# Performance work log

Measured on AMD Instinct MI355X. Metric: run time of the kernel, lower is better.

## Reference

```python
import jax, jax.numpy as jnp
import numpy as np

NB, T, NS, NC = 1024, 128, 12, 4
N = NS + NC  # stacked state+control dim


def setup_inputs() -> dict:
    key = jax.random.key(0)
    ks = jax.random.split(key, 7)
    x_init = jax.random.normal(ks[0], (NB, NS), jnp.float32)
    current_x = jax.random.normal(ks[1], (NB, T, NS), jnp.float32)
    current_u = jax.random.normal(ks[2], (NB, T, NC), jnp.float32)
    # symmetric positive-definite cost Hessian per (batch, t)
    G = 0.1 * jax.random.normal(ks[3], (NB, T, N, N), jnp.float32)
    Q = 0.5 * (G + jnp.swapaxes(G, -1, -2)) + jnp.eye(N, dtype=jnp.float32)
    p = jax.random.normal(ks[4], (NB, T, N), jnp.float32)
    # stable per-step dynamics linearizations
    A = 0.95 * jnp.eye(NS, dtype=jnp.float32) + 0.02 * jax.random.normal(ks[5], (NB, T, NS, NS), jnp.float32)
    Bmat = 0.1 * jax.random.normal(ks[6], (NB, T, NS, NC), jnp.float32)
    time = jnp.arange(T, dtype=jnp.int32)
    return {"x_init": x_init, "current_x": current_x, "current_u": current_u,
            "Q": Q, "p": p, "A": A, "Bmat": Bmat, "time": time}


def _lqr_backward(Q, p, A, Bmat):
    # time-major for scan: (T, NB, ...)
    Qs = jnp.moveaxis(Q, 1, 0)
    ps = jnp.moveaxis(p, 1, 0)
    As = jnp.moveaxis(A, 1, 0)
    Bs = jnp.moveaxis(Bmat, 1, 0)
    nb = Q.shape[0]
    V0 = jnp.zeros((nb, NS, NS), Q.dtype)  # V=0 reproduces the t==T-1 branch
    v0 = jnp.zeros((nb, NS), Q.dtype)

    def step(carry, inp):
        V, v = carry
        Qt0, pt, At, Bt = inp
        F = jnp.concatenate([At, Bt], axis=-1)          # (nb, ns, n)
        FT = jnp.swapaxes(F, -1, -2)                    # (nb, n, ns)
        Qt = Qt0 + FT @ V @ F                           # (nb, n, n)
        qt = pt + jnp.einsum('bsn,bs->bn', F, v)        # F^T v
        Qxx, Qxu = Qt[..., :NS, :NS], Qt[..., :NS, NS:]
        Qux, Quu = Qt[..., NS:, :NS], Qt[..., NS:, NS:]
        qx, qu = qt[..., :NS], qt[..., NS:]
        Quu_inv = jnp.linalg.pinv(Quu)                  # (nb, nc, nc)
        Kt = -(Quu_inv @ Qux)                           # (nb, nc, ns)
        kt = -jnp.einsum('bij,bj->bi', Quu_inv, qu)     # (nb, nc)
        KtT = jnp.swapaxes(Kt, -1, -2)
        Vn = Qxx + Qxu @ Kt + KtT @ Qux + KtT @ Quu @ Kt
        vn = (qx + jnp.einsum('bij,bj->bi', Qxu, kt)
              + jnp.einsum('bij,bj->bi', KtT, qu)
              + jnp.einsum('bij,bj->bi', KtT @ Quu, kt))
        return (Vn, vn), (Kt, kt)

    _, (K, k) = jax.lax.scan(step, (V0, v0), (Qs, ps, As, Bs), reverse=True)
    return jnp.moveaxis(K, 0, 1), jnp.moveaxis(k, 0, 1)


def _lqr_forward(x_init, current_u, Q, p, A, Bmat, K, k):
    Ks = jnp.moveaxis(K, 1, 0)
    ks_ = jnp.moveaxis(k, 1, 0)
    As = jnp.moveaxis(A, 1, 0)
    Bs = jnp.moveaxis(Bmat, 1, 0)
    cus = jnp.moveaxis(current_u, 1, 0)
    Qs = jnp.moveaxis(Q, 1, 0)
    ps = jnp.moveaxis(p, 1, 0)
    nb = x_init.shape[0]
    cost0 = jnp.zeros((nb,), x_init.dtype)

    def step(carry, inp):
        xt, cost = carry
        Kt, kt, At, Bt, cut, Qt, pt = inp
        # NOTE: original module never updates delta_x (stays zero), so delta_u == k_t
        ut = cut + kt
        xut = jnp.concatenate([xt, ut], axis=-1)        # (nb, n)
        xnext = jnp.einsum('bij,bj->bi', At, xt) + jnp.einsum('bij,bj->bi', Bt, ut)
        cost = cost + 0.5 * jnp.einsum('bi,bij,bj->b', xut, Qt, xut) + jnp.sum(xut * pt, axis=-1)
        return (xnext, cost), (xt, ut)

    (_, cost), (xs, us) = jax.lax.scan(step, (x_init, cost0), (Ks, ks_, As, Bs, cus, Qs, ps))
    # xs holds x_0..x_{T-1}, matching return of x[..., 0:-1, :]
    return jnp.moveaxis(xs, 0, 1), jnp.moveaxis(us, 0, 1), cost


def reference(x_init, current_x, current_u, Q, p, A, Bmat, time):
    K, k = _lqr_backward(Q, p, A, Bmat)
    return _lqr_forward(x_init, current_u, Q, p, A, Bmat, K, k)
```

## Files before the change

kernel.cpp:

```cpp
#include <hip/hip_runtime.h>


#define NBQ 1024
#define TT  128

__device__ __forceinline__ float dotf4(float4 a, float4 b) {
  return a.x*b.x + a.y*b.y + a.z*b.z + a.w*b.w;
}
__device__ __forceinline__ float dpp_qx1(float x) {
  return __int_as_float(__builtin_amdgcn_mov_dpp(__float_as_int(x), 0xB1, 0xF, 0xF, true));
}
__device__ __forceinline__ float dpp_qx2(float x) {
  return __int_as_float(__builtin_amdgcn_mov_dpp(__float_as_int(x), 0x4E, 0xF, 0xF, true));
}
template<int Q> __device__ __forceinline__ float4 bcast4(float4 v) {
  float4 r;
  r.x = __int_as_float(__builtin_amdgcn_mov_dpp(__float_as_int(v.x), Q*0x55, 0xF, 0xF, true));
  r.y = __int_as_float(__builtin_amdgcn_mov_dpp(__float_as_int(v.y), Q*0x55, 0xF, 0xF, true));
  r.z = __int_as_float(__builtin_amdgcn_mov_dpp(__float_as_int(v.z), Q*0x55, 0xF, 0xF, true));
  r.w = __int_as_float(__builtin_amdgcn_mov_dpp(__float_as_int(v.w), Q*0x55, 0xF, 0xF, true));
  return r;
}

#define MKS(K, O, MY)  { float4 mk_ = bcast4<O>(MY);                           \
  qt4_.x += gk_[K]*mk_.x; qt4_.y += gk_[K]*mk_.y;                              \
  qt4_.z += gk_[K]*mk_.z; qt4_.w += gk_[K]*mk_.w; }

#define BW_BODY(T_, QV, PV, CV, P0,P1,P2,P3, S0,S1,S2,S3)                      \
{                                                                              \
  const int  t_   = (T_);                                                      \
  const long bt_  = b*TT + t_;                                                 \
  const long btL_ = b*TT + ((t_ >= 4) ? (t_ - 4) : 0);                         \
  float4 qN_ = *(const float4*)(Qg + btL_*256 + qoff);                         \
  const float* fpL_ = lt48 ? (Ag + btL_*144 + l) : (Bg + btL_*48 + bm_);       \
  float fN0_ = fpL_[0], fN1_ = fpL_[fstr_], fN2_ = fpL_[2*fstr_], fN3_ = fpL_[foff3];  \
  float  pN_ = pg[btL_*16 + j];                                                \
  float  cN_ = cug[btL_*4 + q4];                                               \
  float* FTc_ = (t_ & 1) ? FT1 : FT0;                                          \
  float* FTn_ = (t_ & 1) ? FT0 : FT1;                                          \
                     \
  if (lt48)      { FTn_[ba] = P0; FTn_[ba+4] = P1; FTn_[ba+8] = P2; }          \
  else if (lt60) { FTn_[bb] = P0; FTn_[bb+3] = P1; FTn_[bb+6] = P2; FTn_[bb+9] = P3; } \
   \
  const float4* fj4_ = (const float4*)(FTc_ + j*12);                           \
  float4 f0_=fj4_[0], f1_=fj4_[1], f2_=fj4_[2];                                \
  const float4* vrow_ = (const float4*)(Vs + (3*r + dmin)*12);                 \
  float4 mv0_=vrow_[0], mv1_=vrow_[1], mv2_=vrow_[2];                          \
  float4 mw_ = *(const float4*)(vvS + 4*dmin);                                 \
                                      \
  float m0_, m1_, m2_;                                                         \
  { float4 r0_=bcast4<0>(mv0_), r1_=bcast4<0>(mv1_), r2_=bcast4<0>(mv2_);      \
    m0_ = dotf4(r0_,f0_)+dotf4(r1_,f1_)+dotf4(r2_,f2_); }                      \
  { float4 r0_=bcast4<1>(mv0_), r1_=bcast4<1>(mv1_), r2_=bcast4<1>(mv2_);      \
    m1_ = dotf4(r0_,f0_)+dotf4(r1_,f1_)+dotf4(r2_,f2_); }                      \
  { float4 r0_=bcast4<2>(mv0_), r1_=bcast4<2>(mv1_), r2_=bcast4<2>(mv2_);      \
    m2_ = dotf4(r0_,f0_)+dotf4(r1_,f1_)+dotf4(r2_,f2_); }                      \
  msh[(3*r+0)*16 + j] = m0_;                                                   \
  msh[(3*r+1)*16 + j] = m1_;                                                   \
  msh[(3*r+2)*16 + j] = m2_;                                                   \
                \
  float qtv_;                                                                  \
  { float4 w0_=bcast4<0>(mw_), w1_=bcast4<1>(mw_), w2_=bcast4<2>(mw_);         \
    qtv_ = PV + dotf4(w0_,f0_)+dotf4(w1_,f1_)+dotf4(w2_,f2_); }                \
                    \
  float gk_[12] = {f0_.x,f0_.y,f0_.z,f0_.w, f1_.x,f1_.y,f1_.z,f1_.w,           \
                   f2_.x,f2_.y,f2_.z,f2_.w};                                   \
  float4 mys0_ = *(const float4*)(msh + (3*q4+0)*16 + cb4);                    \
  float4 mys1_ = *(const float4*)(msh + (3*q4+1)*16 + cb4);                    \
  float4 mys2_ = *(const float4*)(msh + (3*q4+2)*16 + cb4);                    \
  float4 qt4_ = QV;                                                            \
  MKS(0,0,mys0_) MKS(1,0,mys1_) MKS(2,0,mys2_)                                 \
  MKS(3,1,mys0_) MKS(4,1,mys1_) MKS(5,1,mys2_)                                 \
  MKS(6,2,mys0_) MKS(7,2,mys1_) MKS(8,2,mys2_)                                 \
  MKS(9,3,mys0_) MKS(10,3,mys1_) MKS(11,3,mys2_)                               \
                                            \
  if (j >= 12)           *(float4*)(UxS + (j-12)*16 + cb4) = qt4_;             \
  if (cb == 3 && j < 12) *(float4*)(XuS + j*4) = qt4_;                         \
  if (l >= 12 && l < 16) quS[l-12] = qtv_;                                     \
                                         \
  float4 myquu_ = *(const float4*)(UxS + q4*16 + 12);                          \
  float4 myux_  = *(const float4*)(UxS + q4*16 + cb4);                         \
  float4 quv_   = *(const float4*)quS;                                         \
  float4 xr_    = *(const float4*)(XuS + jc*4);                                \
  float mm_[16];                                                               \
  { float4 t0_=bcast4<0>(myquu_); mm_[0]=t0_.x; mm_[1]=t0_.y; mm_[2]=t0_.z; mm_[3]=t0_.w; \
    float4 t1_=bcast4<1>(myquu_); mm_[4]=t1_.x; mm_[5]=t1_.y; mm_[6]=t1_.z; mm_[7]=t1_.w; \
    float4 t2_=bcast4<2>(myquu_); mm_[8]=t2_.x; mm_[9]=t2_.y; mm_[10]=t2_.z; mm_[11]=t2_.w; \
    float4 t3_=bcast4<3>(myquu_); mm_[12]=t3_.x; mm_[13]=t3_.y; mm_[14]=t3_.z; mm_[15]=t3_.w; } \
  float4 ux0_=bcast4<0>(myux_), ux1_=bcast4<1>(myux_),                         \
         ux2_=bcast4<2>(myux_), ux3_=bcast4<3>(myux_);                         \
                                       \
  float rdp_ = 1.0f/(mm_[0]*mm_[5] - mm_[1]*mm_[1]);                           \
  float pi00_ = mm_[5]*rdp_, pi01_ = -mm_[1]*rdp_, pi11_ = mm_[0]*rdp_;        \
  float w00_ = pi00_*mm_[2] + pi01_*mm_[6];                                    \
  float w01_ = pi00_*mm_[3] + pi01_*mm_[7];                                    \
  float w10_ = pi01_*mm_[2] + pi11_*mm_[6];                                    \
  float w11_ = pi01_*mm_[3] + pi11_*mm_[7];                                    \
  float t00_ = mm_[10] - (mm_[2]*w00_ + mm_[6]*w10_);                          \
  float t01_ = mm_[11] - (mm_[2]*w01_ + mm_[6]*w11_);                          \
  float t11_ = mm_[15] - (mm_[3]*w01_ + mm_[7]*w11_);                          \
  float rdt_ = 1.0f/(t00_*t11_ - t01_*t01_);                                   \
  float ti00_ = t11_*rdt_, ti01_ = -t01_*rdt_, ti11_ = t00_*rdt_;              \
  float u00_ = -(w00_*ti00_ + w01_*ti01_);                                     \
  float u01_ = -(w00_*ti01_ + w01_*ti11_);                                     \
  float u10_ = -(w10_*ti00_ + w11_*ti01_);                                     \
  float u11_ = -(w10_*ti01_ + w11_*ti11_);                                     \
  float i00_ = pi00_ - (u00_*w00_ + u01_*w01_);                                \
  float i01_ = pi01_ - (u00_*w10_ + u01_*w11_);                                \
  float i11_ = pi11_ - (u10_*w10_ + u11_*w11_);                                \
  float inv_[16] = { i00_, i01_, u00_, u01_,                                   \
                     i01_, i11_, u10_, u11_,                                   \
                     u00_, u10_, ti00_, ti01_,                                 \
                     u01_, u11_, ti01_, ti11_ };                               \
  float kt0_ = -(inv_[0] *quv_.x + inv_[1] *quv_.y + inv_[2] *quv_.z + inv_[3] *quv_.w); \
  float kt1_ = -(inv_[4] *quv_.x + inv_[5] *quv_.y + inv_[6] *quv_.z + inv_[7] *quv_.w); \
  float kt2_ = -(inv_[8] *quv_.x + inv_[9] *quv_.y + inv_[10]*quv_.z + inv_[11]*quv_.w); \
  float kt3_ = -(inv_[12]*quv_.x + inv_[13]*quv_.y + inv_[14]*quv_.z + inv_[15]*quv_.w); \
  float4 kc_[4];                                                               \
  _Pragma("unroll")                                                            \
  for (int c_ = 0; c_ < 4; ++c_) {                                             \
    kc_[c_].x = -(inv_[c_*4+0]*ux0_.x + inv_[c_*4+1]*ux1_.x + inv_[c_*4+2]*ux2_.x + inv_[c_*4+3]*ux3_.x); \
    kc_[c_].y = -(inv_[c_*4+0]*ux0_.y + inv_[c_*4+1]*ux1_.y + inv_[c_*4+2]*ux2_.y + inv_[c_*4+3]*ux3_.y); \
    kc_[c_].z = -(inv_[c_*4+0]*ux0_.z + inv_[c_*4+1]*ux1_.z + inv_[c_*4+2]*ux2_.z + inv_[c_*4+3]*ux3_.z); \
    kc_[c_].w = -(inv_[c_*4+0]*ux0_.w + inv_[c_*4+1]*ux1_.w + inv_[c_*4+2]*ux2_.w + inv_[c_*4+3]*ux3_.w); \
  }                                                                            \
  if (j < 12) {                                                                \
    float4 vn4_;                                                               \
    vn4_.x = qt4_.x + xr_.x*kc_[0].x + xr_.y*kc_[1].x + xr_.z*kc_[2].x + xr_.w*kc_[3].x; \
    vn4_.y = qt4_.y + xr_.x*kc_[0].y + xr_.y*kc_[1].y + xr_.z*kc_[2].y + xr_.w*kc_[3].y; \
    vn4_.z = qt4_.z + xr_.x*kc_[0].z + xr_.y*kc_[1].z + xr_.z*kc_[2].z + xr_.w*kc_[3].z; \
    vn4_.w = qt4_.w + xr_.x*kc_[0].w + xr_.y*kc_[1].w + xr_.z*kc_[2].w + xr_.w*kc_[3].w; \
    if (cb < 3) *(float4*)(Vs + j*12 + cb4) = vn4_;                            \
  }                                                                            \
  if (l < 12)                                                                  \
    vvS[l] = qtv_ + xr_.x*kt0_ + xr_.y*kt1_ + xr_.z*kt2_ + xr_.w*kt3_;         \
  float uv_ = CV + ((q4==0)?kt0_:(q4==1)?kt1_:(q4==2)?kt2_:kt3_);              \
  if (l < 4) { us_out[bt_*4 + l] = uv_; uL[t_*4 + l] = uv_; }                  \
  QV = qN_; S0 = fN0_; S1 = fN1_; S2 = fN2_; S3 = fN3_; PV = pN_; CV = cN_;    \
}

__global__ __launch_bounds__(64, 1) void lqr_fused(
    const float* __restrict__ Qg, const float* __restrict__ pg,
    const float* __restrict__ Ag, const float* __restrict__ Bg,
    const float* __restrict__ cug, const float* __restrict__ xinit,
    float* __restrict__ out)
{
  __shared__ __align__(16) float lds[1376];
  float* FT0 = lds;
  float* FT1 = lds + 192;
  float* Vs  = lds + 384;
  float* vvS = lds + 528;
  float* msh = lds + 544;
  float* UxS = lds + 736;
  float* XuS = lds + 800;
  float* quS = lds + 848;
  float* uL  = lds + 864;

  const int l    = threadIdx.x;
  const int j    = l & 15;
  const int r    = l >> 4;
  const int q4   = l & 3;
  const int cb   = l >> 4;
  const int cb4  = cb << 2;
  const int dmin = (q4 < 2) ? q4 : 2;
  const int jc   = (j < 12) ? j : 11;
  const long b   = blockIdx.x;
  const bool lt48 = (l < 48);
  const bool lt60 = (l < 60);
  const int  bm_  = lt48 ? 0 : ((l - 48) % 12);
  const int  fstr_ = lt48 ? 48 : 12;
  const int  foff3 = lt48 ? 96 : 36;
  const int  ba = (l % 12) * 12 + l / 12;
  const int  bb = 144 + ((l - 48) & 3) * 12 + ((l - 48) >> 2);
  const int  qoff = j * 16 + cb4;

  float* xs_out = out;
  float* us_out = out + (long)NBQ*TT*12;
  float* c_out  = out + (long)NBQ*TT*12 + (long)NBQ*TT*4;

  if (j < 12 && cb < 3) *(float4*)(Vs + j*12 + cb4) = make_float4(0.f,0.f,0.f,0.f);
  if (l < 12) vvS[l] = 0.f;

  const long base = b*TT;
  float4 q3v,q2v,q1v,q0v;
  float  p3v,c3v,p2v,c2v,p1v,c1v,p0v,c0v;
  float  f3a,f3b,f3c,f3d, f2a,f2b,f2c,f2d, f1a,f1b,f1c,f1d, f0a,f0b,f0c,f0d;
  {
    long bt;
    bt = base+127; q3v=*(const float4*)(Qg+bt*256+qoff); p3v=pg[bt*16+j]; c3v=cug[bt*4+q4];
    { const float* fp = lt48 ? (Ag+bt*144+l) : (Bg+bt*48+bm_);
      f3a=fp[0]; f3b=fp[fstr_]; f3c=fp[2*fstr_]; f3d=fp[foff3]; }
    bt = base+126; q2v=*(const float4*)(Qg+bt*256+qoff); p2v=pg[bt*16+j]; c2v=cug[bt*4+q4];
    { const float* fp = lt48 ? (Ag+bt*144+l) : (Bg+bt*48+bm_);
      f2a=fp[0]; f2b=fp[fstr_]; f2c=fp[2*fstr_]; f2d=fp[foff3]; }
    bt = base+125; q1v=*(const float4*)(Qg+bt*256+qoff); p1v=pg[bt*16+j]; c1v=cug[bt*4+q4];
    { const float* fp = lt48 ? (Ag+bt*144+l) : (Bg+bt*48+bm_);
      f1a=fp[0]; f1b=fp[fstr_]; f1c=fp[2*fstr_]; f1d=fp[foff3]; }
    bt = base+124; q0v=*(const float4*)(Qg+bt*256+qoff); p0v=pg[bt*16+j]; c0v=cug[bt*4+q4];
    { const float* fp = lt48 ? (Ag+bt*144+l) : (Bg+bt*48+bm_);
      f0a=fp[0]; f0b=fp[fstr_]; f0c=fp[2*fstr_]; f0d=fp[foff3]; }
  }
  if (lt48)      { FT1[ba] = f3a; FT1[ba+4] = f3b; FT1[ba+8] = f3c; }
  else if (lt60) { FT1[bb] = f3a; FT1[bb+3] = f3b; FT1[bb+6] = f3c; FT1[bb+9] = f3d; }

  #pragma unroll 1
  for (int tb = TT-1; tb >= 3; tb -= 4) {
    BW_BODY(tb,   q3v, p3v, c3v,  f2a,f2b,f2c,f2d,  f3a,f3b,f3c,f3d)
    BW_BODY(tb-1, q2v, p2v, c2v,  f1a,f1b,f1c,f1d,  f2a,f2b,f2c,f2d)
    BW_BODY(tb-2, q1v, p1v, c1v,  f0a,f0b,f0c,f0d,  f1a,f1b,f1c,f1d)
    BW_BODY(tb-3, q0v, p0v, c0v,  f3a,f3b,f3c,f3d,  f0a,f0b,f0c,f0d)
  }

  const int i4  = l >> 2;
  const int c0f = q4 << 2;
  const int i4c = (i4 < 12) ? i4 : 11;
  const int sl0 = (c0f+0)<<2, sl1 = (c0f+1)<<2, sl2 = (c0f+2)<<2, sl3 = (c0f+3)<<2;
  float s = xinit[b*12 + i4c];
  float cacc = 0.f;

  const long bt0 = base;
  float4 qfA = *(const float4*)(Qg + bt0*256 + 4*l);
  float4 ffA = (q4 < 3) ? *(const float4*)(Ag + bt0*144 + i4c*12 + c0f)
                        : *(const float4*)(Bg + bt0*48  + i4c*4);
  float  pfA = pg[bt0*16 + i4];
  float4 qfB = *(const float4*)(Qg + (bt0+1)*256 + 4*l);
  float4 ffB = (q4 < 3) ? *(const float4*)(Ag + (bt0+1)*144 + i4c*12 + c0f)
                        : *(const float4*)(Bg + (bt0+1)*48  + i4c*4);
  float  pfB = pg[(bt0+1)*16 + i4];
  float4 qfC = *(const float4*)(Qg + (bt0+2)*256 + 4*l);
  float4 ffC = (q4 < 3) ? *(const float4*)(Ag + (bt0+2)*144 + i4c*12 + c0f)
                        : *(const float4*)(Bg + (bt0+2)*48  + i4c*4);
  float  pfC = pg[(bt0+2)*16 + i4];

  #pragma unroll 1
  for (int t = 0; t < TT; ++t) {
    const long btp = bt0 + ((t+3 < TT-1) ? t+3 : TT-1);
    float4 qfD = *(const float4*)(Qg + btp*256 + 4*l);
    float4 ffD = (q4 < 3) ? *(const float4*)(Ag + btp*144 + i4c*12 + c0f)
                          : *(const float4*)(Bg + btp*48  + i4c*4);
    float  pfD = pg[btp*16 + i4];

    float4 u4 = *(const float4*)(uL + t*4);

    float4 xg;
    xg.x = __shfl(s, sl0, 64); xg.y = __shfl(s, sl1, 64);
    xg.z = __shfl(s, sl2, 64); xg.w = __shfl(s, sl3, 64);
    float4 xuq = (q4 < 3) ? xg : u4;
    float xui = (i4 < 12) ? s
              : (i4 == 12) ? u4.x : (i4 == 13) ? u4.y : (i4 == 14) ? u4.z : u4.w;

    if (q4 == 0 && i4 < 12) xs_out[(bt0+t)*12 + i4] = s;

    cacc += 0.5f * xui * dotf4(qfA, xuq);
    if (q4 == 0) cacc += xui * pfA;

    float zx = dotf4(ffA, xuq);
    zx += dpp_qx1(zx);
    zx += dpp_qx2(zx);
    s = zx;

    qfA = qfB; ffA = ffB; pfA = pfB;
    qfB = qfC; ffB = ffC; pfB = pfC;
    qfC = qfD; ffC = ffD; pfC = pfD;
  }

  cacc += __shfl_xor(cacc, 32, 64);
  cacc += __shfl_xor(cacc, 16, 64);
  cacc += __shfl_xor(cacc, 8, 64);
  cacc += __shfl_xor(cacc, 4, 64);
  cacc += dpp_qx2(cacc);
  cacc += dpp_qx1(cacc);
  if (l == 0) c_out[b] = cacc;
}

extern "C" void kernel_launch(void* const* d_in, const int* in_sizes, int n_in,
                              void* d_out, int out_size, void* d_ws, size_t ws_size,
                              hipStream_t stream) {
  const float* xinit = (const float*)d_in[0];
  const float* cu = (const float*)d_in[2];
  const float* Q  = (const float*)d_in[3];
  const float* p  = (const float*)d_in[4];
  const float* A  = (const float*)d_in[5];
  const float* Bm = (const float*)d_in[6];
  float* out = (float*)d_out;

  lqr_fused<<<dim3(NBQ), dim3(64), 0, stream>>>(Q, p, A, Bm, cu, xinit, out);
}
```

Measured before the change: 383.1 us.

## Split fused LQR kernel into separate backward and forward kernels

Splits the single fused kernel, which ran the backward Riccati sweep and then the forward rollout in one block, into two kernels. The forward kernel reads the controls back from global output instead of LDS and deepens its prefetch pipeline to four steps ahead. This lowers LDS use in the backward kernel and simplifies each kernel's register footprint. It costs a second launch and a global round trip for the controls, and the forward pass rereads Q, A and B from memory, probably from L2.

Result: slower. 399.2 us (+4.2%).

```diff
diff --git a/kernel.cpp b/kernel.cpp
--- a/kernel.cpp
+++ b/kernel.cpp
@@ -38,16 +38,13 @@
   float  cN_ = cug[btL_*4 + q4];                                               \
   float* FTc_ = (t_ & 1) ? FT1 : FT0;                                          \
   float* FTn_ = (t_ & 1) ? FT0 : FT1;                                          \
-                     \
   if (lt48)      { FTn_[ba] = P0; FTn_[ba+4] = P1; FTn_[ba+8] = P2; }          \
   else if (lt60) { FTn_[bb] = P0; FTn_[bb+3] = P1; FTn_[bb+6] = P2; FTn_[bb+9] = P3; } \
-   \
   const float4* fj4_ = (const float4*)(FTc_ + j*12);                           \
   float4 f0_=fj4_[0], f1_=fj4_[1], f2_=fj4_[2];                                \
   const float4* vrow_ = (const float4*)(Vs + (3*r + dmin)*12);                 \
   float4 mv0_=vrow_[0], mv1_=vrow_[1], mv2_=vrow_[2];                          \
   float4 mw_ = *(const float4*)(vvS + 4*dmin);                                 \
-                                      \
   float m0_, m1_, m2_;                                                         \
   { float4 r0_=bcast4<0>(mv0_), r1_=bcast4<0>(mv1_), r2_=bcast4<0>(mv2_);      \
     m0_ = dotf4(r0_,f0_)+dotf4(r1_,f1_)+dotf4(r2_,f2_); }                      \
@@ -58,11 +55,9 @@
   msh[(3*r+0)*16 + j] = m0_;                                                   \
   msh[(3*r+1)*16 + j] = m1_;                                                   \
   msh[(3*r+2)*16 + j] = m2_;                                                   \
-                \
   float qtv_;                                                                  \
   { float4 w0_=bcast4<0>(mw_), w1_=bcast4<1>(mw_), w2_=bcast4<2>(mw_);         \
     qtv_ = PV + dotf4(w0_,f0_)+dotf4(w1_,f1_)+dotf4(w2_,f2_); }                \
-                    \
   float gk_[12] = {f0_.x,f0_.y,f0_.z,f0_.w, f1_.x,f1_.y,f1_.z,f1_.w,           \
                    f2_.x,f2_.y,f2_.z,f2_.w};                                   \
   float4 mys0_ = *(const float4*)(msh + (3*q4+0)*16 + cb4);                    \
@@ -73,11 +68,9 @@
   MKS(3,1,mys0_) MKS(4,1,mys1_) MKS(5,1,mys2_)                                 \
   MKS(6,2,mys0_) MKS(7,2,mys1_) MKS(8,2,mys2_)                                 \
   MKS(9,3,mys0_) MKS(10,3,mys1_) MKS(11,3,mys2_)                               \
-                                            \
   if (j >= 12)           *(float4*)(UxS + (j-12)*16 + cb4) = qt4_;             \
   if (cb == 3 && j < 12) *(float4*)(XuS + j*4) = qt4_;                         \
   if (l >= 12 && l < 16) quS[l-12] = qtv_;                                     \
-                                         \
   float4 myquu_ = *(const float4*)(UxS + q4*16 + 12);                          \
   float4 myux_  = *(const float4*)(UxS + q4*16 + cb4);                         \
   float4 quv_   = *(const float4*)quS;                                         \
@@ -89,7 +82,6 @@
     float4 t3_=bcast4<3>(myquu_); mm_[12]=t3_.x; mm_[13]=t3_.y; mm_[14]=t3_.z; mm_[15]=t3_.w; } \
   float4 ux0_=bcast4<0>(myux_), ux1_=bcast4<1>(myux_),                         \
          ux2_=bcast4<2>(myux_), ux3_=bcast4<3>(myux_);                         \
-                                       \
   float rdp_ = 1.0f/(mm_[0]*mm_[5] - mm_[1]*mm_[1]);                           \
   float pi00_ = mm_[5]*rdp_, pi01_ = -mm_[1]*rdp_, pi11_ = mm_[0]*rdp_;        \
   float w00_ = pi00_*mm_[2] + pi01_*mm_[6];                                    \
@@ -135,17 +127,16 @@
   if (l < 12)                                                                  \
     vvS[l] = qtv_ + xr_.x*kt0_ + xr_.y*kt1_ + xr_.z*kt2_ + xr_.w*kt3_;         \
   float uv_ = CV + ((q4==0)?kt0_:(q4==1)?kt1_:(q4==2)?kt2_:kt3_);              \
-  if (l < 4) { us_out[bt_*4 + l] = uv_; uL[t_*4 + l] = uv_; }                  \
+  if (l < 4) us_out[bt_*4 + l] = uv_;                                          \
   QV = qN_; S0 = fN0_; S1 = fN1_; S2 = fN2_; S3 = fN3_; PV = pN_; CV = cN_;    \
 }
 
-__global__ __launch_bounds__(64, 1) void lqr_fused(
+__global__ __launch_bounds__(64, 1) void lqr_bw(
     const float* __restrict__ Qg, const float* __restrict__ pg,
     const float* __restrict__ Ag, const float* __restrict__ Bg,
-    const float* __restrict__ cug, const float* __restrict__ xinit,
-    float* __restrict__ out)
+    const float* __restrict__ cug, float* __restrict__ us_out)
 {
-  __shared__ __align__(16) float lds[1376];
+  __shared__ __align__(16) float lds[864];
   float* FT0 = lds;
   float* FT1 = lds + 192;
   float* Vs  = lds + 384;
@@ -154,7 +145,6 @@
   float* UxS = lds + 736;
   float* XuS = lds + 800;
   float* quS = lds + 848;
-  float* uL  = lds + 864;
 
   const int l    = threadIdx.x;
   const int j    = l & 15;
@@ -174,10 +164,6 @@
   const int  bb = 144 + ((l - 48) & 3) * 12 + ((l - 48) >> 2);
   const int  qoff = j * 16 + cb4;
 
-  float* xs_out = out;
-  float* us_out = out + (long)NBQ*TT*12;
-  float* c_out  = out + (long)NBQ*TT*12 + (long)NBQ*TT*4;
-
   if (j < 12 && cb < 3) *(float4*)(Vs + j*12 + cb4) = make_float4(0.f,0.f,0.f,0.f);
   if (l < 12) vvS[l] = 0.f;
 
@@ -210,38 +196,57 @@
     BW_BODY(tb-2, q1v, p1v, c1v,  f0a,f0b,f0c,f0d,  f1a,f1b,f1c,f1d)
     BW_BODY(tb-3, q0v, p0v, c0v,  f3a,f3b,f3c,f3d,  f0a,f0b,f0c,f0d)
   }
-
+}
+
+__global__ __launch_bounds__(64, 1) void lqr_fw(
+    const float* __restrict__ Qg, const float* __restrict__ pg,
+    const float* __restrict__ Ag, const float* __restrict__ Bg,
+    const float* __restrict__ xinit, float* __restrict__ out)
+{
+  const int l   = threadIdx.x;
+  const int q4  = l & 3;
   const int i4  = l >> 2;
   const int c0f = q4 << 2;
   const int i4c = (i4 < 12) ? i4 : 11;
   const int sl0 = (c0f+0)<<2, sl1 = (c0f+1)<<2, sl2 = (c0f+2)<<2, sl3 = (c0f+3)<<2;
+  const long b  = blockIdx.x;
+
+  float* xs_out = out;
+  const float* us_in = out + (long)NBQ*TT*12;
+  float* c_out  = out + (long)NBQ*TT*12 + (long)NBQ*TT*4;
+
   float s = xinit[b*12 + i4c];
   float cacc = 0.f;
 
-  const long bt0 = base;
-  float4 qfA = *(const float4*)(Qg + bt0*256 + 4*l);
-  float4 ffA = (q4 < 3) ? *(const float4*)(Ag + bt0*144 + i4c*12 + c0f)
-                        : *(const float4*)(Bg + bt0*48  + i4c*4);
-  float  pfA = pg[bt0*16 + i4];
-  float4 qfB = *(const float4*)(Qg + (bt0+1)*256 + 4*l);
-  float4 ffB = (q4 < 3) ? *(const float4*)(Ag + (bt0+1)*144 + i4c*12 + c0f)
-                        : *(const float4*)(Bg + (bt0+1)*48  + i4c*4);
-  float  pfB = pg[(bt0+1)*16 + i4];
-  float4 qfC = *(const float4*)(Qg + (bt0+2)*256 + 4*l);
-  float4 ffC = (q4 < 3) ? *(const float4*)(Ag + (bt0+2)*144 + i4c*12 + c0f)
-                        : *(const float4*)(Bg + (bt0+2)*48  + i4c*4);
-  float  pfC = pg[(bt0+2)*16 + i4];
+  const long bt0 = b*TT;
+  float4 qfA, ffA, ufA, qfB, ffB, ufB, qfC, ffC, ufC, qfD, ffD, ufD;
+  float  pfA, pfB, pfC, pfD;
+  {
+    long bt;
+    bt = bt0+0; qfA=*(const float4*)(Qg+bt*256+4*l); pfA=pg[bt*16+i4];
+    ffA=(q4<3)?*(const float4*)(Ag+bt*144+i4c*12+c0f):*(const float4*)(Bg+bt*48+i4c*4);
+    ufA=*(const float4*)(us_in+bt*4);
+    bt = bt0+1; qfB=*(const float4*)(Qg+bt*256+4*l); pfB=pg[bt*16+i4];
+    ffB=(q4<3)?*(const float4*)(Ag+bt*144+i4c*12+c0f):*(const float4*)(Bg+bt*48+i4c*4);
+    ufB=*(const float4*)(us_in+bt*4);
+    bt = bt0+2; qfC=*(const float4*)(Qg+bt*256+4*l); pfC=pg[bt*16+i4];
+    ffC=(q4<3)?*(const float4*)(Ag+bt*144+i4c*12+c0f):*(const float4*)(Bg+bt*48+i4c*4);
+    ufC=*(const float4*)(us_in+bt*4);
+    bt = bt0+3; qfD=*(const float4*)(Qg+bt*256+4*l); pfD=pg[bt*16+i4];
+    ffD=(q4<3)?*(const float4*)(Ag+bt*144+i4c*12+c0f):*(const float4*)(Bg+bt*48+i4c*4);
+    ufD=*(const float4*)(us_in+bt*4);
+  }
 
   #pragma unroll 1
   for (int t = 0; t < TT; ++t) {
-    const long btp = bt0 + ((t+3 < TT-1) ? t+3 : TT-1);
-    float4 qfD = *(const float4*)(Qg + btp*256 + 4*l);
-    float4 ffD = (q4 < 3) ? *(const float4*)(Ag + btp*144 + i4c*12 + c0f)
+    const long btp = bt0 + ((t+4 < TT-1) ? t+4 : TT-1);
+    float4 qfE = *(const float4*)(Qg + btp*256 + 4*l);
+    float4 ffE = (q4 < 3) ? *(const float4*)(Ag + btp*144 + i4c*12 + c0f)
                           : *(const float4*)(Bg + btp*48  + i4c*4);
-    float  pfD = pg[btp*16 + i4];
-
-    float4 u4 = *(const float4*)(uL + t*4);
-
+    float  pfE = pg[btp*16 + i4];
+    float4 ufE = *(const float4*)(us_in + btp*4);
+
+    float4 u4 = ufA;
     float4 xg;
     xg.x = __shfl(s, sl0, 64); xg.y = __shfl(s, sl1, 64);
     xg.z = __shfl(s, sl2, 64); xg.w = __shfl(s, sl3, 64);
@@ -259,9 +264,10 @@
     zx += dpp_qx2(zx);
     s = zx;
 
-    qfA = qfB; ffA = ffB; pfA = pfB;
-    qfB = qfC; ffB = ffC; pfB = pfC;
-    qfC = qfD; ffC = ffD; pfC = pfD;
+    qfA = qfB; ffA = ffB; pfA = pfB; ufA = ufB;
+    qfB = qfC; ffB = ffC; pfB = pfC; ufB = ufC;
+    qfC = qfD; ffC = ffD; pfC = pfD; ufC = ufD;
+    qfD = qfE; ffD = ffE; pfD = pfE; ufD = ufE;
   }
 
   cacc += __shfl_xor(cacc, 32, 64);
@@ -283,6 +289,8 @@
   const float* A  = (const float*)d_in[5];
   const float* Bm = (const float*)d_in[6];
   float* out = (float*)d_out;
-
-  lqr_fused<<<dim3(NBQ), dim3(64), 0, stream>>>(Q, p, A, Bm, cu, xinit, out);
-}
+  float* us_out = out + (long)NBQ*TT*12;
+
+  lqr_bw<<<dim3(NBQ), dim3(64), 0, stream>>>(Q, p, A, Bm, cu, us_out);
+  lqr_fw<<<dim3(NBQ), dim3(64), 0, stream>>>(Q, p, A, Bm, xinit, out);
+}
```
